# Performance work log

Hardware: AMD Instinct MI355X
Metric: run time of the kernel (lower is better)

Reference implementation:

```python
import jax, jax.numpy as jnp
import numpy as np

BS, J, L, D = 32, 4, 512, 768  # batch, entity sentences, max_bert_len, bert_embed_dim
K = 4                          # num_entity_per_sentence; J*K == num_candidates == 16
OUT = 256                      # entity_final_output_dim


def setup_inputs() -> dict:
    key = jax.random.key(0)
    k1, k2, k3, k4 = jax.random.split(key, 4)
    zipped_entity = jax.random.normal(k1, (BS, J, L, D), dtype=jnp.float32)
    # strictly increasing separator indices per (b, j); spans are [last+1, sep)
    steps = jax.random.randint(k2, (BS, J, K), 5, 60)
    entity_token_sep_idx = 1 + jnp.cumsum(steps, axis=-1)  # values < 1+4*60 < L
    W = jax.random.normal(k3, (D, OUT), dtype=jnp.float32) * 0.02
    b = jax.random.normal(k4, (OUT,), dtype=jnp.float32) * 0.02
    return {"zipped_entity": zipped_entity,
            "entity_token_sep_idx": entity_token_sep_idx,
            "W": W, "b": b}


def reference(zipped_entity, entity_token_sep_idx, W, b):
    # Ragged per-entity span mean-pool, vectorized via a span mask, then Linear.
    sep = entity_token_sep_idx                                    # [bs, J, K]
    starts = jnp.concatenate([jnp.ones_like(sep[..., :1]), sep[..., :-1] + 1], axis=-1)
    ends = sep                                                    # exclusive
    t = jnp.arange(L)                                             # token positions
    # mask[b,j,k,l] = 1 if token l belongs to entity k of sentence j
    mask = ((t[None, None, None, :] >= starts[..., None]) &
            (t[None, None, None, :] < ends[..., None])).astype(zipped_entity.dtype)
    sums = jnp.einsum('bjkl,bjld->bjkd', mask, zipped_entity)     # [bs, J, K, D]
    counts = (ends - starts).astype(zipped_entity.dtype)[..., None]
    pooled = sums / counts                                        # mean over span
    bs = zipped_entity.shape[0]
    # entity_idx = k + j*K -> reshape [bs, J, K, D] to [bs, num_candidates, D]
    encoded_entity = pooled.reshape(bs, J * K, D)
    return encoded_entity @ W + b                                 # final Linear
```

## Files before the change

### kernel.cpp

```cpp
#include <hip/hip_runtime.h>
#include <hip/hip_bf16.h>

#define BS  32
#define J   4
#define L   512
#define D   768
#define K   4
#define OUT 256

typedef float f4 __attribute__((ext_vector_type(4)));

__global__ __launch_bounds__(128) void pool_kernel(
    const float* __restrict__ Z,
    const int*   __restrict__ sep,
    float*       __restrict__ ws)
{
    const int blk  = blockIdx.x;
    const int e    = blk >> 2, q = blk & 3;
    const int sent = e >> 2,  k = e & 3;
    const int end   = sep[sent * K + k];
    const int prev  = (k == 0) ? 0 : sep[sent * K + k - 1];
    const int start = prev + 1;
    const float inv = 1.0f / (float)(end - start);

    const int w    = threadIdx.x >> 6;
    const int lane = threadIdx.x & 63;
    const float* zbase = Z + (size_t)sent * L * D + lane * 4;

    f4 a0={0,0,0,0}, a1={0,0,0,0}, a2={0,0,0,0};
    f4 c0={0,0,0,0}, c1={0,0,0,0}, c2={0,0,0,0};

    int l = start + q + 4 * w;
    for (; l + 8 < end; l += 16) {
        const float* r0 = zbase + (size_t)l * D;
        const float* r1 = zbase + (size_t)(l + 8) * D;
        a0 += *(const f4*)(r0);       a1 += *(const f4*)(r0 + 256);
        a2 += *(const f4*)(r0 + 512);
        c0 += *(const f4*)(r1);       c1 += *(const f4*)(r1 + 256);
        c2 += *(const f4*)(r1 + 512);
    }
    if (l < end) {
        const float* r0 = zbase + (size_t)l * D;
        a0 += *(const f4*)(r0);       a1 += *(const f4*)(r0 + 256);
        a2 += *(const f4*)(r0 + 512);
    }
    a0 += c0; a1 += c1; a2 += c2;

    __shared__ float part[2][D];
    *(f4*)&part[w][lane*4]       = a0;
    *(f4*)&part[w][lane*4 + 256] = a1;
    *(f4*)&part[w][lane*4 + 512] = a2;
    __syncthreads();

    float* dst = ws + ((size_t)(sent * 4 + q) * K + k) * D;
    for (int i = threadIdx.x; i < 192; i += 128) {
        f4 s = *(const f4*)&part[0][i*4] + *(const f4*)&part[1][i*4];
        s *= inv;
        *(f4*)&dst[i*4] = s;
    }
}

__global__ __launch_bounds__(512) void gemm_kernel(
    const float* __restrict__ ws,
    const float* __restrict__ W,
    const float* __restrict__ bias,
    float*       __restrict__ out)
{
    const int g  = blockIdx.x >> 2;
    const int cq = blockIdx.x & 3;

    __shared__ float p[K * D];
    __shared__ float red[32][K][64];
    {
        const f4* a = (const f4*)(ws + (size_t)g * 4 * K * D);
        for (int i = threadIdx.x; i < (K * D) / 4; i += 512) {
            f4 v = a[i] + a[i + 768] + a[i + 2 * 768] + a[i + 3 * 768];
            *(f4*)&p[i * 4] = v;
        }
    }
    __syncthreads();

    const int w    = threadIdx.x >> 6;
    const int lane = threadIdx.x & 63;
    const int dg   = lane >> 4;
    const int cl   = lane & 15;
    const int colbase = cq * 64 + cl * 4;
    const int dbase   = w * 96 + dg;

    f4 acc0={0,0,0,0}, acc1={0,0,0,0}, acc2={0,0,0,0}, acc3={0,0,0,0};
    #pragma unroll 8
    for (int i = 0; i < 24; ++i) {
        const int d = dbase + 4 * i;
        f4 wv = *(const f4*)&W[(size_t)d * OUT + colbase];
        acc0 += p[0 * D + d] * wv;
        acc1 += p[1 * D + d] * wv;
        acc2 += p[2 * D + d] * wv;
        acc3 += p[3 * D + d] * wv;
    }

    const int r = w * 4 + dg;
    *(f4*)&red[r][0][cl * 4] = acc0;
    *(f4*)&red[r][1][cl * 4] = acc1;
    *(f4*)&red[r][2][cl * 4] = acc2;
    *(f4*)&red[r][3][cl * 4] = acc3;
    __syncthreads();

    if (threadIdx.x < 256) {
        const int e2  = threadIdx.x >> 6;
        const int col = threadIdx.x & 63;
        float s = bias[cq * 64 + col];
        #pragma unroll
        for (int rr = 0; rr < 32; ++rr) s += red[rr][e2][col];
        out[(size_t)(g * K + e2) * OUT + cq * 64 + col] = s;
    }
}

extern "C" void kernel_launch(void* const* d_in, const int* in_sizes, int n_in,
                              void* d_out, int out_size, void* d_ws, size_t ws_size,
                              hipStream_t stream) {
    const float* Z    = (const float*)d_in[0];
    const int*   sep  = (const int*)d_in[1];
    const float* W    = (const float*)d_in[2];
    const float* bias = (const float*)d_in[3];
    float*       out  = (float*)d_out;
    float*       ws   = (float*)d_ws;

    pool_kernel<<<4 * BS * J * K, 128, 0, stream>>>(Z, sep, ws);
    gemm_kernel<<<BS * J * K, 512, 0, stream>>>(ws, W, bias, out);
}
```

Before: 23.59 us.

## Split pooling by fixed token chunks per sentence, classifying tokens into entities

The pooling kernel now assigns each block a fixed 32-token chunk of a sentence, instead of a quarter of one entity's span. Each warp routes every token row to one of four per-entity accumulators by comparing it against the separator indices. This is meant to balance work across blocks regardless of ragged span lengths and to cut per-block overhead. The mean division moves into the GEMM kernel, which now sums eight chunk partials instead of four. In exchange the kernel holds more accumulator registers, does a three-stage shared-memory reduction, and writes partials even for chunks past the last span, which doubles the workspace traffic.

```diff
diff --git a/kernel.cpp b/kernel.cpp
--- a/kernel.cpp
+++ b/kernel.cpp
@@ -7,61 +7,97 @@
 #define D   768
 #define K   4
 #define OUT 256
+#define NCHUNK 8
+#define CHTOK  32
 
 typedef float f4 __attribute__((ext_vector_type(4)));
 
-__global__ __launch_bounds__(128) void pool_kernel(
+#define CHAIN(LV, V0, V1, V2)                                              \
+    if ((LV) < s0)                     { A00+=V0; A01+=V1; A02+=V2; }      \
+    else if ((LV) > s0 && (LV) < s1)   { A10+=V0; A11+=V1; A12+=V2; }      \
+    else if ((LV) > s1 && (LV) < s2)   { A20+=V0; A21+=V1; A22+=V2; }      \
+    else if ((LV) > s2)                { A30+=V0; A31+=V1; A32+=V2; }
+
+#define DUMP(dst) {                                                        \
+    *(f4*)&(dst)[0*D + 0*256 + lane*4] = A00;                              \
+    *(f4*)&(dst)[0*D + 1*256 + lane*4] = A01;                              \
+    *(f4*)&(dst)[0*D + 2*256 + lane*4] = A02;                              \
+    *(f4*)&(dst)[1*D + 0*256 + lane*4] = A10;                              \
+    *(f4*)&(dst)[1*D + 1*256 + lane*4] = A11;                              \
+    *(f4*)&(dst)[1*D + 2*256 + lane*4] = A12;                              \
+    *(f4*)&(dst)[2*D + 0*256 + lane*4] = A20;                              \
+    *(f4*)&(dst)[2*D + 1*256 + lane*4] = A21;                              \
+    *(f4*)&(dst)[2*D + 2*256 + lane*4] = A22;                              \
+    *(f4*)&(dst)[3*D + 0*256 + lane*4] = A30;                              \
+    *(f4*)&(dst)[3*D + 1*256 + lane*4] = A31;                              \
+    *(f4*)&(dst)[3*D + 2*256 + lane*4] = A32; }
+
+#define ADDL(src) {                                                        \
+    A00 += *(const f4*)&(src)[0*D + 0*256 + lane*4];                       \
+    A01 += *(const f4*)&(src)[0*D + 1*256 + lane*4];                       \
+    A02 += *(const f4*)&(src)[0*D + 2*256 + lane*4];                       \
+    A10 += *(const f4*)&(src)[1*D + 0*256 + lane*4];                       \
+    A11 += *(const f4*)&(src)[1*D + 1*256 + lane*4];                       \
+    A12 += *(const f4*)&(src)[1*D + 2*256 + lane*4];                       \
+    A20 += *(const f4*)&(src)[2*D + 0*256 + lane*4];                       \
+    A21 += *(const f4*)&(src)[2*D + 1*256 + lane*4];                       \
+    A22 += *(const f4*)&(src)[2*D + 2*256 + lane*4];                       \
+    A30 += *(const f4*)&(src)[3*D + 0*256 + lane*4];                       \
+    A31 += *(const f4*)&(src)[3*D + 1*256 + lane*4];                       \
+    A32 += *(const f4*)&(src)[3*D + 2*256 + lane*4]; }
+
+__global__ __launch_bounds__(256) void pool_kernel(
     const float* __restrict__ Z,
     const int*   __restrict__ sep,
     float*       __restrict__ ws)
 {
-    const int blk  = blockIdx.x;
-    const int e    = blk >> 2, q = blk & 3;
-    const int sent = e >> 2,  k = e & 3;
-    const int end   = sep[sent * K + k];
-    const int prev  = (k == 0) ? 0 : sep[sent * K + k - 1];
-    const int start = prev + 1;
-    const float inv = 1.0f / (float)(end - start);
-
+    const int blk = blockIdx.x;
+    const int g   = blk >> 3;
+    const int c   = blk & 7;
+    const int s0 = sep[g*K+0], s1 = sep[g*K+1], s2 = sep[g*K+2], s3 = sep[g*K+3];
     const int w    = threadIdx.x >> 6;
     const int lane = threadIdx.x & 63;
-    const float* zbase = Z + (size_t)sent * L * D + lane * 4;
+    const int base = 1 + CHTOK * c;
+    const int lend = min(base + CHTOK, s3);
+    const float* zbase = Z + (size_t)g * L * D + lane * 4;
 
-    f4 a0={0,0,0,0}, a1={0,0,0,0}, a2={0,0,0,0};
-    f4 c0={0,0,0,0}, c1={0,0,0,0}, c2={0,0,0,0};
+    f4 A00={0,0,0,0},A01={0,0,0,0},A02={0,0,0,0};
+    f4 A10={0,0,0,0},A11={0,0,0,0},A12={0,0,0,0};
+    f4 A20={0,0,0,0},A21={0,0,0,0},A22={0,0,0,0};
+    f4 A30={0,0,0,0},A31={0,0,0,0},A32={0,0,0,0};
 
-    int l = start + q + 4 * w;
-    for (; l + 8 < end; l += 16) {
+    int l = base + w;
+    for (; l + 4 < lend; l += 8) {
         const float* r0 = zbase + (size_t)l * D;
-        const float* r1 = zbase + (size_t)(l + 8) * D;
-        a0 += *(const f4*)(r0);       a1 += *(const f4*)(r0 + 256);
-        a2 += *(const f4*)(r0 + 512);
-        c0 += *(const f4*)(r1);       c1 += *(const f4*)(r1 + 256);
-        c2 += *(const f4*)(r1 + 512);
+        const float* r1 = r0 + 4 * D;
+        f4 u0=*(const f4*)r0, u1=*(const f4*)(r0+256), u2=*(const f4*)(r0+512);
+        f4 v0=*(const f4*)r1, v1=*(const f4*)(r1+256), v2=*(const f4*)(r1+512);
+        CHAIN(l,     u0, u1, u2);
+        CHAIN(l + 4, v0, v1, v2);
     }
-    if (l < end) {
+    if (l < lend) {
         const float* r0 = zbase + (size_t)l * D;
-        a0 += *(const f4*)(r0);       a1 += *(const f4*)(r0 + 256);
-        a2 += *(const f4*)(r0 + 512);
+        f4 u0=*(const f4*)r0, u1=*(const f4*)(r0+256), u2=*(const f4*)(r0+512);
+        CHAIN(l, u0, u1, u2);
     }
-    a0 += c0; a1 += c1; a2 += c2;
 
-    __shared__ float part[2][D];
-    *(f4*)&part[w][lane*4]       = a0;
-    *(f4*)&part[w][lane*4 + 256] = a1;
-    *(f4*)&part[w][lane*4 + 512] = a2;
+    __shared__ float red[2][K * D];
+    if (w >= 2) DUMP(red[w - 2]);
     __syncthreads();
-
-    float* dst = ws + ((size_t)(sent * 4 + q) * K + k) * D;
-    for (int i = threadIdx.x; i < 192; i += 128) {
-        f4 s = *(const f4*)&part[0][i*4] + *(const f4*)&part[1][i*4];
-        s *= inv;
-        *(f4*)&dst[i*4] = s;
+    if (w < 2)  ADDL(red[w]);
+    __syncthreads();
+    if (w == 1) DUMP(red[0]);
+    __syncthreads();
+    if (w == 0) {
+        ADDL(red[0]);
+        float* dst = ws + (size_t)blk * (K * D);
+        DUMP(dst);
     }
 }
 
 __global__ __launch_bounds__(512) void gemm_kernel(
     const float* __restrict__ ws,
+    const int*   __restrict__ sep,
     const float* __restrict__ W,
     const float* __restrict__ bias,
     float*       __restrict__ out)
@@ -71,11 +107,23 @@
 
     __shared__ float p[K * D];
     __shared__ float red[32][K][64];
+    __shared__ float sinv[K];
+
+    if (threadIdx.x < K) {
+        const int e    = threadIdx.x;
+        const int end  = sep[g*K + e];
+        const int prev = (e == 0) ? 0 : sep[g*K + e - 1];
+        sinv[e] = 1.0f / (float)(end - prev - 1);
+    }
+    __syncthreads();
+
     {
-        const f4* a = (const f4*)(ws + (size_t)g * 4 * K * D);
+        const f4* a = (const f4*)(ws + (size_t)g * NCHUNK * K * D);
         for (int i = threadIdx.x; i < (K * D) / 4; i += 512) {
-            f4 v = a[i] + a[i + 768] + a[i + 2 * 768] + a[i + 3 * 768];
-            *(f4*)&p[i * 4] = v;
+            f4 s = a[i]          + a[i + 768]     + a[i + 2*768] + a[i + 3*768]
+                 + a[i + 4*768]  + a[i + 5*768]   + a[i + 6*768] + a[i + 7*768];
+            const int e = (i >= 192) + (i >= 384) + (i >= 576);
+            *(f4*)&p[i * 4] = s * sinv[e];
         }
     }
     __syncthreads();
@@ -125,6 +173,6 @@
     float*       out  = (float*)d_out;
     float*       ws   = (float*)d_ws;
 
-    pool_kernel<<<4 * BS * J * K, 128, 0, stream>>>(Z, sep, ws);
-    gemm_kernel<<<BS * J * K, 512, 0, stream>>>(ws, W, bias, out);
+    pool_kernel<<<BS * J * NCHUNK, 256, 0, stream>>>(Z, sep, ws);
+    gemm_kernel<<<BS * J * K, 512, 0, stream>>>(ws, sep, W, bias, out);
 }
```

After: 34.07 us. +44.4%, slower.

## Fuse span pooling and linear into one kernel with last-block atomic handoff

Applied to the files above, without the earlier changes.

Merges the pooling and GEMM kernels into a single launch. Each entity is pooled by two 256-thread blocks, and the second block to finish (detected with an agent-scope atomic counter) sums the halves and computes that entity's 256 outputs against W. This removes the second kernel launch and the inter-kernel gap. It adds a memset launch to zero the counters, and the GEMM step now reads the W matrix separately for each entity instead of sharing W reads across four entities per block.

```diff
diff --git a/kernel.cpp b/kernel.cpp
--- a/kernel.cpp
+++ b/kernel.cpp
@@ -10,108 +10,99 @@
 
 typedef float f4 __attribute__((ext_vector_type(4)));
 
-__global__ __launch_bounds__(128) void pool_kernel(
+__global__ __launch_bounds__(256, 4) void fused_kernel(
     const float* __restrict__ Z,
     const int*   __restrict__ sep,
-    float*       __restrict__ ws)
-{
-    const int blk  = blockIdx.x;
-    const int e    = blk >> 2, q = blk & 3;
-    const int sent = e >> 2,  k = e & 3;
-    const int end   = sep[sent * K + k];
-    const int prev  = (k == 0) ? 0 : sep[sent * K + k - 1];
-    const int start = prev + 1;
-    const float inv = 1.0f / (float)(end - start);
-
-    const int w    = threadIdx.x >> 6;
-    const int lane = threadIdx.x & 63;
-    const float* zbase = Z + (size_t)sent * L * D + lane * 4;
-
-    f4 a0={0,0,0,0}, a1={0,0,0,0}, a2={0,0,0,0};
-    f4 c0={0,0,0,0}, c1={0,0,0,0}, c2={0,0,0,0};
-
-    int l = start + q + 4 * w;
-    for (; l + 8 < end; l += 16) {
-        const float* r0 = zbase + (size_t)l * D;
-        const float* r1 = zbase + (size_t)(l + 8) * D;
-        a0 += *(const f4*)(r0);       a1 += *(const f4*)(r0 + 256);
-        a2 += *(const f4*)(r0 + 512);
-        c0 += *(const f4*)(r1);       c1 += *(const f4*)(r1 + 256);
-        c2 += *(const f4*)(r1 + 512);
-    }
-    if (l < end) {
-        const float* r0 = zbase + (size_t)l * D;
-        a0 += *(const f4*)(r0);       a1 += *(const f4*)(r0 + 256);
-        a2 += *(const f4*)(r0 + 512);
-    }
-    a0 += c0; a1 += c1; a2 += c2;
-
-    __shared__ float part[2][D];
-    *(f4*)&part[w][lane*4]       = a0;
-    *(f4*)&part[w][lane*4 + 256] = a1;
-    *(f4*)&part[w][lane*4 + 512] = a2;
-    __syncthreads();
-
-    float* dst = ws + ((size_t)(sent * 4 + q) * K + k) * D;
-    for (int i = threadIdx.x; i < 192; i += 128) {
-        f4 s = *(const f4*)&part[0][i*4] + *(const f4*)&part[1][i*4];
-        s *= inv;
-        *(f4*)&dst[i*4] = s;
-    }
-}
-
-__global__ __launch_bounds__(512) void gemm_kernel(
-    const float* __restrict__ ws,
     const float* __restrict__ W,
     const float* __restrict__ bias,
-    float*       __restrict__ out)
+    float*       __restrict__ out,
+    float*       __restrict__ ws,
+    int*         __restrict__ cnt)
 {
-    const int g  = blockIdx.x >> 2;
-    const int cq = blockIdx.x & 3;
+    __shared__ float part[4][D];
+    __shared__ float pg[D];
+    __shared__ f4    red[4][64];
+    __shared__ int   flag;
 
-    __shared__ float p[K * D];
-    __shared__ float red[32][K][64];
+    const int blk  = blockIdx.x;
+    const int e    = blk >> 1, h = blk & 1;
+    const int sent = e >> 2,  k = e & 3;
+    const int tid  = threadIdx.x;
+    const int w    = tid >> 6;
+    const int lane = tid & 63;
+
     {
-        const f4* a = (const f4*)(ws + (size_t)g * 4 * K * D);
-        for (int i = threadIdx.x; i < (K * D) / 4; i += 512) {
-            f4 v = a[i] + a[i + 768] + a[i + 2 * 768] + a[i + 3 * 768];
-            *(f4*)&p[i * 4] = v;
+        const int end   = sep[sent * K + k];
+        const int prev  = (k == 0) ? 0 : sep[sent * K + k - 1];
+        const int start = prev + 1;
+        const float inv = 1.0f / (float)(end - start);
+        const float* zbase = Z + (size_t)sent * L * D + lane * 4;
+
+        f4 a0={0,0,0,0}, a1={0,0,0,0}, a2={0,0,0,0};
+        f4 c0={0,0,0,0}, c1={0,0,0,0}, c2={0,0,0,0};
+
+        int l = start + h + 2 * w;
+        for (; l + 8 < end; l += 16) {
+            const float* r0 = zbase + (size_t)l * D;
+            const float* r1 = zbase + (size_t)(l + 8) * D;
+            a0 += *(const f4*)(r0);       a1 += *(const f4*)(r0 + 256);
+            a2 += *(const f4*)(r0 + 512);
+            c0 += *(const f4*)(r1);       c1 += *(const f4*)(r1 + 256);
+            c2 += *(const f4*)(r1 + 512);
+        }
+        if (l < end) {
+            const float* r0 = zbase + (size_t)l * D;
+            a0 += *(const f4*)(r0);       a1 += *(const f4*)(r0 + 256);
+            a2 += *(const f4*)(r0 + 512);
+        }
+        a0 += c0; a1 += c1; a2 += c2;
+
+        *(f4*)&part[w][lane*4]       = a0;
+        *(f4*)&part[w][lane*4 + 256] = a1;
+        *(f4*)&part[w][lane*4 + 512] = a2;
+        __syncthreads();
+
+        if (tid < 192) {
+            f4 s = {0,0,0,0};
+            #pragma unroll
+            for (int ww = 0; ww < 4; ++ww) s += *(const f4*)&part[ww][tid*4];
+            s *= inv;
+            *(f4*)&ws[((size_t)e * 2 + h) * D + tid*4] = s;
         }
     }
     __syncthreads();
 
-    const int w    = threadIdx.x >> 6;
-    const int lane = threadIdx.x & 63;
-    const int dg   = lane >> 4;
-    const int cl   = lane & 15;
-    const int colbase = cq * 64 + cl * 4;
-    const int dbase   = w * 96 + dg;
+    if (tid == 0) {
+        flag = __hip_atomic_fetch_add(&cnt[e], 1, __ATOMIC_ACQ_REL,
+                                      __HIP_MEMORY_SCOPE_AGENT);
+    }
+    __syncthreads();
+    if (flag != 1) return;
 
-    f4 acc0={0,0,0,0}, acc1={0,0,0,0}, acc2={0,0,0,0}, acc3={0,0,0,0};
-    #pragma unroll 8
-    for (int i = 0; i < 24; ++i) {
-        const int d = dbase + 4 * i;
-        f4 wv = *(const f4*)&W[(size_t)d * OUT + colbase];
-        acc0 += p[0 * D + d] * wv;
-        acc1 += p[1 * D + d] * wv;
-        acc2 += p[2 * D + d] * wv;
-        acc3 += p[3 * D + d] * wv;
+    {
+        const f4* aa = (const f4*)(ws + (size_t)e * 2 * D);
+        if (tid < 192) {
+            f4 v = aa[tid] + aa[tid + 192];
+            *(f4*)&pg[tid * 4] = v;
+        }
     }
-
-    const int r = w * 4 + dg;
-    *(f4*)&red[r][0][cl * 4] = acc0;
-    *(f4*)&red[r][1][cl * 4] = acc1;
-    *(f4*)&red[r][2][cl * 4] = acc2;
-    *(f4*)&red[r][3][cl * 4] = acc3;
     __syncthreads();
 
-    if (threadIdx.x < 256) {
-        const int e2  = threadIdx.x >> 6;
-        const int col = threadIdx.x & 63;
-        float s = bias[cq * 64 + col];
-        #pragma unroll
-        for (int rr = 0; rr < 32; ++rr) s += red[rr][e2][col];
-        out[(size_t)(g * K + e2) * OUT + cq * 64 + col] = s;
+    f4 acc = {0,0,0,0};
+    const int colb = lane * 4;
+    #pragma unroll 8
+    for (int i = 0; i < 192; ++i) {
+        const int d = w + 4 * i;
+        f4 wv = *(const f4*)&W[(size_t)d * OUT + colb];
+        acc += pg[d] * wv;
+    }
+    red[w][lane] = acc;
+    __syncthreads();
+
+    if (tid < 64) {
+        f4 o = red[0][tid] + red[1][tid] + red[2][tid] + red[3][tid]
+             + *(const f4*)&bias[tid * 4];
+        *(f4*)&out[(size_t)e * OUT + tid * 4] = o;
     }
 }
 
@@ -124,7 +115,8 @@
     const float* bias = (const float*)d_in[3];
     float*       out  = (float*)d_out;
     float*       ws   = (float*)d_ws;
+    int*         cnt  = (int*)(ws + 512 * 2 * D);
 
-    pool_kernel<<<4 * BS * J * K, 128, 0, stream>>>(Z, sep, ws);
-    gemm_kernel<<<BS * J * K, 512, 0, stream>>>(ws, W, bias, out);
+    hipMemsetAsync(cnt, 0, 512 * sizeof(int), stream);
+    fused_kernel<<<2 * BS * J * K, 256, 0, stream>>>(Z, sep, W, bias, out, ws, cnt);
 }
```

Measured after the change: 76.40 us. +223.9%, slower.
